# Kernel tuning notes

Measured on AMD Instinct MI355X. Metric: run time of the kernel, lower is better.

The kernel has to match this reference:

```python
import jax, jax.numpy as jnp
import numpy as np

D_MODEL = 1024
N_HEADS = 16
D_K = D_MODEL // N_HEADS
D_HIDDEN = 2048
LN_EPS = 1e-5


def setup_inputs() -> dict:
    key = jax.random.key(0)
    ks = jax.random.split(key, 16)
    s = 0.02
    inp = {
        'x': jax.random.normal(ks[0], (4, 2048, D_MODEL), dtype=jnp.float32),
        'Wq': jax.random.normal(ks[1], (D_MODEL, D_MODEL), dtype=jnp.float32) * s,
        'bq': jnp.zeros((D_MODEL,), jnp.float32),
        'Wk': jax.random.normal(ks[2], (D_MODEL, D_MODEL), dtype=jnp.float32) * s,
        'bk': jnp.zeros((D_MODEL,), jnp.float32),
        'Wv': jax.random.normal(ks[3], (D_MODEL, D_MODEL), dtype=jnp.float32) * s,
        'bv': jnp.zeros((D_MODEL,), jnp.float32),
        'Wo': jax.random.normal(ks[4], (D_MODEL, D_MODEL), dtype=jnp.float32) * s,
        'bo': jnp.zeros((D_MODEL,), jnp.float32),
        'ln1_g': jnp.ones((D_MODEL,), jnp.float32),
        'ln1_b': jnp.zeros((D_MODEL,), jnp.float32),
        'ln2_g': jnp.ones((D_MODEL,), jnp.float32),
        'ln2_b': jnp.zeros((D_MODEL,), jnp.float32),
        'W1': jax.random.normal(ks[5], (2 * D_HIDDEN, D_MODEL), dtype=jnp.float32) * s,
        'b1': jnp.zeros((2 * D_HIDDEN,), jnp.float32),
        'W2': jax.random.normal(ks[6], (D_MODEL, D_HIDDEN), dtype=jnp.float32) * s,
        'b2': jnp.zeros((D_MODEL,), jnp.float32),
    }
    return inp


def _layernorm(x, g, b):
    mu = jnp.mean(x, axis=-1, keepdims=True)
    var = jnp.mean(jnp.square(x - mu), axis=-1, keepdims=True)
    return (x - mu) * jax.lax.rsqrt(var + LN_EPS) * g + b


def _attention(xn, Wq, bq, Wk, bk, Wv, bv, Wo, bo):
    B, S, _ = xn.shape
    def split_heads(t):  # [B,S,D] -> [B,H,S,Dk]
        return t.reshape(B, S, N_HEADS, D_K).transpose(0, 2, 1, 3)
    Q = split_heads(xn @ Wq.T + bq)
    K = split_heads(xn @ Wk.T + bk)
    V = split_heads(xn @ Wv.T + bv)
    scores = jnp.einsum('bhqd,bhkd->bhqk', Q, K) / jnp.float32(D_K ** 0.5)
    attn = jax.nn.softmax(scores, axis=-1)  # torch code does max-sub + softmax (same math)
    ctx = jnp.einsum('bhqk,bhkd->bhqd', attn, V)
    ctx = ctx.transpose(0, 2, 1, 3).reshape(B, S, D_MODEL)
    return ctx @ Wo.T + bo


def reference(x, Wq, bq, Wk, bk, Wv, bv, Wo, bo, ln1_g, ln1_b, ln2_g, ln2_b, W1, b1, W2, b2):
    # pre-norm attention block
    xn = _layernorm(x, ln1_g, ln1_b)
    x = x + _attention(xn, Wq, bq, Wk, bk, Wv, bv, Wo, bo)
    # pre-norm ReGLU FFN
    xn = _layernorm(x, ln2_g, ln2_b)
    h = xn @ W1.T + b1
    a, b_ = jnp.split(h, 2, axis=-1)
    h = jax.nn.relu(a) * b_
    x = x + (h @ W2.T + b2)
    return x
```

## Files before the change

kernel.cpp:

```cpp
#include <hip/hip_runtime.h>
#include <hip/hip_bf16.h>

typedef __attribute__((ext_vector_type(8))) short short8;
typedef __attribute__((ext_vector_type(4))) float floatx4;

#define LN_EPS 1e-5f
#define EXP2_SCALE 0.18033688011112042f

__device__ __forceinline__ float b2f(unsigned short u) {
    union { float f; unsigned int i; } x; x.i = ((unsigned int)u) << 16; return x.f;
}
__device__ __forceinline__ unsigned short f2b(float f) {
    union { float f; unsigned int i; } x; x.f = f;
    unsigned int r = x.i + 0x7fffu + ((x.i >> 16) & 1u);
    return (unsigned short)(r >> 16);
}
__device__ __forceinline__ float to_f(unsigned short u) { return b2f(u); }
__device__ __forceinline__ float to_f(float f) { return f; }
__device__ __forceinline__ unsigned int pk_bf16(float a, float b) {
    union { float f; unsigned int i; } xa, xb; xa.f = a; xb.f = b;
    return (xa.i >> 16) | (xb.i & 0xffff0000u);
}

__device__ __forceinline__ void async16(const unsigned short* g, unsigned short* l) {
    __builtin_amdgcn_global_load_lds(
        (const __attribute__((address_space(1))) unsigned int*)g,
        (__attribute__((address_space(3))) unsigned int*)l, 16, 0, 0);
}

template<typename T>
__device__ __forceinline__ void ln_row(const T* __restrict__ xr, const float* __restrict__ g,
                                       const float* __restrict__ bb, unsigned short* __restrict__ outr,
                                       float* red)
{
    const int tid = threadIdx.x;
    float v[4];
#pragma unroll
    for (int i = 0; i < 4; i++) v[i] = to_f(xr[tid + i * 256]);
    float s  = v[0] + v[1] + v[2] + v[3];
    float sq = v[0]*v[0] + v[1]*v[1] + v[2]*v[2] + v[3]*v[3];
#pragma unroll
    for (int o = 32; o >= 1; o >>= 1) {
        s  += __shfl_xor(s,  o, 64);
        sq += __shfl_xor(sq, o, 64);
    }
    const int wave = tid >> 6, lane = tid & 63;
    if (lane == 0) { red[wave] = s; red[4 + wave] = sq; }
    __syncthreads();
    s  = red[0] + red[1] + red[2] + red[3];
    sq = red[4] + red[5] + red[6] + red[7];
    const float mu  = s * (1.0f / 1024.0f);
    const float var = sq * (1.0f / 1024.0f) - mu * mu;
    const float rs  = rsqrtf(var + LN_EPS);
#pragma unroll
    for (int i = 0; i < 4; i++) {
        int c = tid + i * 256;
        outr[c] = f2b((v[i] - mu) * rs * g[c] + bb[c]);
    }
}

__global__ __launch_bounds__(256)
void prep_kernel(const float* __restrict__ Wq, const float* __restrict__ Wk,
                 const float* __restrict__ Wv, const float* __restrict__ Wo,
                 const float* __restrict__ W1, const float* __restrict__ W2,
                 unsigned short* __restrict__ wdst,
                 const float* __restrict__ x, const float* __restrict__ ln1g,
                 const float* __restrict__ ln1b, unsigned short* __restrict__ xn)
{
    __shared__ float red[8];
    if (blockIdx.x < 5120) {
        const size_t i = (size_t)(blockIdx.x * 256 + threadIdx.x) * 8;
        const float* src; size_t off;
        if (i < 4194304) {
            int w = (int)(i >> 20);
            src = (w == 0) ? Wq : (w == 1) ? Wk : (w == 2) ? Wv : Wo;
            off = i & 1048575;
        } else if (i < 8388608) { src = W1; off = i - 4194304; }
        else                    { src = W2; off = i - 8388608; }
        float4 a = *reinterpret_cast<const float4*>(src + off);
        float4 b = *reinterpret_cast<const float4*>(src + off + 4);
        short8 r;
        r[0] = (short)f2b(a.x); r[1] = (short)f2b(a.y);
        r[2] = (short)f2b(a.z); r[3] = (short)f2b(a.w);
        r[4] = (short)f2b(b.x); r[5] = (short)f2b(b.y);
        r[6] = (short)f2b(b.z); r[7] = (short)f2b(b.w);
        *reinterpret_cast<short8*>(wdst + i) = r;
    } else {
        const int row = blockIdx.x - 5120;
        ln_row<float>(x + (size_t)row * 1024, ln1g, ln1b, xn + (size_t)row * 1024, red);
    }
}

__global__ __launch_bounds__(256)
void ln_kernel(const unsigned short* __restrict__ x, const float* __restrict__ g,
               const float* __restrict__ bb, unsigned short* __restrict__ out)
{
    __shared__ float red[8];
    const int row = blockIdx.x;
    ln_row<unsigned short>(x + (size_t)row * 1024, g, bb, out + (size_t)row * 1024, red);
}

template<int EPI>
__global__ __launch_bounds__(256, 3)
void gemm_nt(const unsigned short* __restrict__ A, const unsigned short* __restrict__ B,
             const float* __restrict__ bias, const void* __restrict__ res,
             void* __restrict__ C, int M, int N, int K)
{
    __shared__ unsigned short As[128 * 64];
    __shared__ unsigned short Bs[128 * 64];
    const int m0 = blockIdx.y * 128, n0 = blockIdx.x * 128;
    const int tid = threadIdx.x, wave = tid >> 6, lane = tid & 63;
    const int wm = (wave >> 1) * 64, wn = (wave & 1) * 64;
    const int lrow = lane & 15, quad = lane >> 4;
    const int srow = wave * 32 + (lane >> 3);
    const int scol = (((lane & 7) ^ ((lane >> 3) & 7)) << 3);
    const int ca0 = (quad ^ (lrow & 7)) << 3;
    const int ca1 = ((quad + 4) ^ (lrow & 7)) << 3;

    floatx4 acc[4][4] = {};
    const unsigned short* gA = A + (size_t)(m0 + srow) * K + scol;
    const unsigned short* gB = B + (size_t)(n0 + srow) * K + scol;
    unsigned short* lA = &As[(wave * 32) * 64];
    unsigned short* lB = &Bs[(wave * 32) * 64];

    for (int k0 = 0; k0 < K; k0 += 64) {
        __syncthreads();
#pragma unroll
        for (int r = 0; r < 4; r++) {
            async16(gA + k0 + (size_t)(r * 8) * K, lA + r * 8 * 64);
            async16(gB + k0 + (size_t)(r * 8) * K, lB + r * 8 * 64);
        }
        __syncthreads();
#pragma unroll
        for (int ks = 0; ks < 2; ks++) {
            const int ca = ks ? ca1 : ca0;
            short8 af[4], bf[4];
#pragma unroll
            for (int i = 0; i < 4; i++)
                af[i] = *reinterpret_cast<const short8*>(&As[(wm + i * 16 + lrow) * 64 + ca]);
#pragma unroll
            for (int j = 0; j < 4; j++)
                bf[j] = *reinterpret_cast<const short8*>(&Bs[(wn + j * 16 + lrow) * 64 + ca]);
#pragma unroll
            for (int i = 0; i < 4; i++)
#pragma unroll
                for (int j = 0; j < 4; j++)
                    acc[i][j] = __builtin_amdgcn_mfma_f32_16x16x32_bf16(af[i], bf[j], acc[i][j], 0, 0, 0);
        }
    }

#pragma unroll
    for (int i = 0; i < 4; i++) {
        int rb = m0 + wm + i * 16 + quad * 4;
#pragma unroll
        for (int j = 0; j < 4; j++) {
            int col = n0 + wn + j * 16 + lrow;
            float bv = bias[col];
#pragma unroll
            for (int r = 0; r < 4; r++) {
                size_t idx = (size_t)(rb + r) * N + col;
                float v = acc[i][j][r] + bv;
                if (EPI == 1) {
                    v += ((const float*)res)[idx];
                    ((unsigned short*)C)[idx] = f2b(v);
                } else {
                    v += b2f(((const unsigned short*)res)[idx]);
                    ((float*)C)[idx] = v;
                }
            }
        }
    }
}

__global__ __launch_bounds__(256, 3)
void gemm_qkv(const unsigned short* __restrict__ A, const unsigned short* __restrict__ Wqkv,
              const float* __restrict__ bq, const float* __restrict__ bk, const float* __restrict__ bv,
              unsigned short* __restrict__ QK, unsigned short* __restrict__ Vt)
{
    __shared__ unsigned short As[128 * 64];
    __shared__ unsigned short Bs[128 * 64];
    const int part = blockIdx.x >> 3;
    const int m0 = blockIdx.y * 128, n0 = (blockIdx.x & 7) * 128;
    const int tid = threadIdx.x, wave = tid >> 6, lane = tid & 63;
    const int wm = (wave >> 1) * 64, wn = (wave & 1) * 64;
    const int lrow = lane & 15, quad = lane >> 4;
    const int srow = wave * 32 + (lane >> 3);
    const int scol = (((lane & 7) ^ ((lane >> 3) & 7)) << 3);
    const int ca0 = (quad ^ (lrow & 7)) << 3;
    const int ca1 = ((quad + 4) ^ (lrow & 7)) << 3;
    const unsigned short* B = Wqkv + (size_t)part * 1048576;
    const float* bias = (part == 0) ? bq : (part == 1) ? bk : bv;

    floatx4 acc[4][4] = {};
    const unsigned short* gA = A + (size_t)(m0 + srow) * 1024 + scol;
    const unsigned short* gB = B + (size_t)(n0 + srow) * 1024 + scol;
    unsigned short* lA = &As[(wave * 32) * 64];
    unsigned short* lB = &Bs[(wave * 32) * 64];

    for (int k0 = 0; k0 < 1024; k0 += 64) {
        __syncthreads();
#pragma unroll
        for (int r = 0; r < 4; r++) {
            async16(gA + k0 + (size_t)(r * 8) * 1024, lA + r * 8 * 64);
            async16(gB + k0 + (size_t)(r * 8) * 1024, lB + r * 8 * 64);
        }
        __syncthreads();
#pragma unroll
        for (int ks = 0; ks < 2; ks++) {
            const int ca = ks ? ca1 : ca0;
            short8 af[4], bf[4];
#pragma unroll
            for (int i = 0; i < 4; i++)
                af[i] = *reinterpret_cast<const short8*>(&As[(wm + i * 16 + lrow) * 64 + ca]);
#pragma unroll
            for (int j = 0; j < 4; j++)
                bf[j] = *reinterpret_cast<const short8*>(&Bs[(wn + j * 16 + lrow) * 64 + ca]);
#pragma unroll
            for (int i = 0; i < 4; i++)
#pragma unroll
                for (int j = 0; j < 4; j++)
                    acc[i][j] = __builtin_amdgcn_mfma_f32_16x16x32_bf16(af[i], bf[j], acc[i][j], 0, 0, 0);
        }
    }

#pragma unroll
    for (int i = 0; i < 4; i++) {
        int rb = m0 + wm + i * 16 + quad * 4;
#pragma unroll
        for (int j = 0; j < 4; j++) {
            int col = n0 + wn + j * 16 + lrow;
            float bv2 = bias[col];
            if (part == 0) {
#pragma unroll
                for (int r = 0; r < 4; r++)
                    QK[(size_t)(rb + r) * 1024 + col] = f2b((acc[i][j][r] + bv2) * EXP2_SCALE);
            } else if (part == 1) {
                unsigned short* dst = QK + 8388608;
#pragma unroll
                for (int r = 0; r < 4; r++)
                    dst[(size_t)(rb + r) * 1024 + col] = f2b(acc[i][j][r] + bv2);
            } else {
                int b = rb >> 11, spos = rb & 2047;
                int h = col >> 6, d = col & 63;
                unsigned short* dst = Vt + (((size_t)(b * 16 + h) * 64 + d) << 11) + spos;
                unsigned int u01 = pk_bf16(acc[i][j][0] + bv2, acc[i][j][1] + bv2);
                u01 = (unsigned int)f2b(acc[i][j][0] + bv2) | ((unsigned int)f2b(acc[i][j][1] + bv2) << 16);
                unsigned int u23 = (unsigned int)f2b(acc[i][j][2] + bv2) | ((unsigned int)f2b(acc[i][j][3] + bv2) << 16);
                *reinterpret_cast<uint2*>(dst) = make_uint2(u01, u23);
            }
        }
    }
}

__global__ __launch_bounds__(256, 2)
void gemm_w1_reglu(const unsigned short* __restrict__ A, const unsigned short* __restrict__ B,
                   const float* __restrict__ bias, unsigned short* __restrict__ G)
{
    __shared__ unsigned short As[128 * 64];
    __shared__ unsigned short B0s[128 * 64];
    __shared__ unsigned short B1s[128 * 64];
    const int m0 = blockIdx.y * 128, n0 = blockIdx.x * 128;
    const int tid = threadIdx.x, wave = tid >> 6, lane = tid & 63;
    const int wm = (wave >> 1) * 64, wn = (wave & 1) * 64;
    const int lrow = lane & 15, quad = lane >> 4;
    const int srow = wave * 32 + (lane >> 3);
    const int scol = (((lane & 7) ^ ((lane >> 3) & 7)) << 3);
    const int ca0 = (quad ^ (lrow & 7)) << 3;
    const int ca1 = ((quad + 4) ^ (lrow & 7)) << 3;

    floatx4 acca[4][4] = {};
    floatx4 accb[4][4] = {};
    const unsigned short* gA  = A + (size_t)(m0 + srow) * 1024 + scol;
    const unsigned short* gB0 = B + (size_t)(n0 + srow) * 1024 + scol;
    const unsigned short* gB1 = B + (size_t)(2048 + n0 + srow) * 1024 + scol;
    unsigned short* lA  = &As [(wave * 32) * 64];
    unsigned short* lB0 = &B0s[(wave * 32) * 64];
    unsigned short* lB1 = &B1s[(wave * 32) * 64];

    for (int k0 = 0; k0 < 1024; k0 += 64) {
        __syncthreads();
#pragma unroll
        for (int r = 0; r < 4; r++) {
            async16(gA  + k0 + (size_t)(r * 8) * 1024, lA  + r * 8 * 64);
            async16(gB0 + k0 + (size_t)(r * 8) * 1024, lB0 + r * 8 * 64);
            async16(gB1 + k0 + (size_t)(r * 8) * 1024, lB1 + r * 8 * 64);
        }
        __syncthreads();
#pragma unroll
        for (int ks = 0; ks < 2; ks++) {
            const int ca = ks ? ca1 : ca0;
            short8 af[4], b0[4], b1[4];
#pragma unroll
            for (int i = 0; i < 4; i++)
                af[i] = *reinterpret_cast<const short8*>(&As[(wm + i * 16 + lrow) * 64 + ca]);
#pragma unroll
            for (int j = 0; j < 4; j++) {
                b0[j] = *reinterpret_cast<const short8*>(&B0s[(wn + j * 16 + lrow) * 64 + ca]);
                b1[j] = *reinterpret_cast<const short8*>(&B1s[(wn + j * 16 + lrow) * 64 + ca]);
            }
#pragma unroll
            for (int i = 0; i < 4; i++)
#pragma unroll
                for (int j = 0; j < 4; j++) {
                    acca[i][j] = __builtin_amdgcn_mfma_f32_16x16x32_bf16(af[i], b0[j], acca[i][j], 0, 0, 0);
                    accb[i][j] = __builtin_amdgcn_mfma_f32_16x16x32_bf16(af[i], b1[j], accb[i][j], 0, 0, 0);
                }
        }
    }

#pragma unroll
    for (int i = 0; i < 4; i++) {
        int rb = m0 + wm + i * 16 + quad * 4;
#pragma unroll
        for (int j = 0; j < 4; j++) {
            int col = n0 + wn + j * 16 + lrow;
            float ba = bias[col], bb2 = bias[2048 + col];
#pragma unroll
            for (int r = 0; r < 4; r++) {
                float va = acca[i][j][r] + ba;
                float vb = accb[i][j][r] + bb2;
                G[(size_t)(rb + r) * 2048 + col] = f2b(fmaxf(va, 0.0f) * vb);
            }
        }
    }
}

__global__ __launch_bounds__(256, 4)
void attn_kernel(const unsigned short* __restrict__ Qm, const unsigned short* __restrict__ Km,
                 const unsigned short* __restrict__ Vt, unsigned short* __restrict__ ctx)
{
    __shared__ unsigned short Ks[64 * 64];
    __shared__ unsigned short Vs[64 * 64];
    __shared__ unsigned short Ps[4][32][72];

    const int tid = threadIdx.x, wave = tid >> 6, lane = tid & 63;
    const int lrow = lane & 15, quad = lane >> 4;
    const int qb = blockIdx.x, bh = blockIdx.y;
    const size_t base  = (size_t)(bh >> 4) * 2048 * 1024 + (size_t)(bh & 15) * 64;
    const size_t vbase = (size_t)bh * 131072;
    const int q0 = qb * 128 + wave * 32;
    const int g_sub = (lane >> 3);
    const int g_col = (((lane & 7) ^ (g_sub & 7)) << 3);
    const int ca0 = (quad ^ (lrow & 7)) << 3;
    const int ca1 = ((quad + 4) ^ (lrow & 7)) << 3;

    short8 qf[2][2];
#pragma unroll
    for (int m = 0; m < 2; m++) {
        const unsigned short* qp = Qm + base + (size_t)(q0 + m * 16 + lrow) * 1024 + quad * 8;
        qf[m][0] = *reinterpret_cast<const short8*>(qp);
        qf[m][1] = *reinterpret_cast<const short8*>(qp + 32);
    }

    floatx4 o[2][4] = {};
    float li[2] = {0.f, 0.f};

    for (int t = 0; t < 32; t++) {
        const int k0 = t * 64;
        __syncthreads();
#pragma unroll
        for (int r = 0; r < 2; r++) {
            int krow = wave * 16 + r * 8 + g_sub;
            async16(Km + base + (size_t)(k0 + krow) * 1024 + g_col, &Ks[(wave * 16 + r * 8) * 64]);
            async16(Vt + vbase + (size_t)krow * 2048 + k0 + g_col,  &Vs[(wave * 16 + r * 8) * 64]);
        }
        __syncthreads();

        short8 kf0[4], kf1[4];
#pragma unroll
        for (int j = 0; j < 4; j++) {
            kf0[j] = *reinterpret_cast<const short8*>(&Ks[(j * 16 + lrow) * 64 + ca0]);
            kf1[j] = *reinterpret_cast<const short8*>(&Ks[(j * 16 + lrow) * 64 + ca1]);
        }
        floatx4 s4t[2][4] = {};
#pragma unroll
        for (int m = 0; m < 2; m++)
#pragma unroll
            for (int j = 0; j < 4; j++) {
                s4t[m][j] = __builtin_amdgcn_mfma_f32_16x16x32_bf16(kf0[j], qf[m][0], s4t[m][j], 0, 0, 0);
                s4t[m][j] = __builtin_amdgcn_mfma_f32_16x16x32_bf16(kf1[j], qf[m][1], s4t[m][j], 0, 0, 0);
            }

#pragma unroll
        for (int m = 0; m < 2; m++) {
            float acc = 0.f;
#pragma unroll
            for (int j = 0; j < 4; j++) {
                float p0 = __builtin_amdgcn_exp2f(s4t[m][j][0]);
                float p1 = __builtin_amdgcn_exp2f(s4t[m][j][1]);
                float p2 = __builtin_amdgcn_exp2f(s4t[m][j][2]);
                float p3 = __builtin_amdgcn_exp2f(s4t[m][j][3]);
                acc += (p0 + p1) + (p2 + p3);
                uint2 pk = make_uint2(pk_bf16(p0, p1), pk_bf16(p2, p3));
                *reinterpret_cast<uint2*>(&Ps[wave][m * 16 + lrow][j * 16 + quad * 4]) = pk;
            }
            li[m] += acc;
        }
        __asm__ volatile("s_waitcnt lgkmcnt(0)" ::: "memory");

        short8 pf[2][2];
#pragma unroll
        for (int m = 0; m < 2; m++) {
            pf[m][0] = *reinterpret_cast<const short8*>(&Ps[wave][m * 16 + lrow][quad * 8]);
            pf[m][1] = *reinterpret_cast<const short8*>(&Ps[wave][m * 16 + lrow][32 + quad * 8]);
        }
#pragma unroll
        for (int jj = 0; jj < 4; jj++) {
            short8 vf0 = *reinterpret_cast<const short8*>(&Vs[(jj * 16 + lrow) * 64 + ca0]);
            short8 vf1 = *reinterpret_cast<const short8*>(&Vs[(jj * 16 + lrow) * 64 + ca1]);
#pragma unroll
            for (int m = 0; m < 2; m++) {
                o[m][jj] = __builtin_amdgcn_mfma_f32_16x16x32_bf16(pf[m][0], vf0, o[m][jj], 0, 0, 0);
                o[m][jj] = __builtin_amdgcn_mfma_f32_16x16x32_bf16(pf[m][1], vf1, o[m][jj], 0, 0, 0);
            }
        }
    }

#pragma unroll
    for (int m = 0; m < 2; m++) {
        float l = li[m];
        l += __shfl_xor(l, 16, 64);
        l += __shfl_xor(l, 32, 64);
        float inv = 1.0f / l;
#pragma unroll
        for (int r = 0; r < 4; r++) {
            float invr = __shfl(inv, quad * 4 + r, 64);
            int srow = q0 + m * 16 + quad * 4 + r;
#pragma unroll
            for (int jj = 0; jj < 4; jj++)
                ctx[base + (size_t)srow * 1024 + jj * 16 + lrow] = f2b(o[m][jj][r] * invr);
        }
    }
}

extern "C" void kernel_launch(void* const* d_in, const int* in_sizes, int n_in,
                              void* d_out, int out_size, void* d_ws, size_t ws_size,
                              hipStream_t stream) {
    const float* x    = (const float*)d_in[0];
    const float* Wq   = (const float*)d_in[1];
    const float* bq   = (const float*)d_in[2];
    const float* Wk   = (const float*)d_in[3];
    const float* bk   = (const float*)d_in[4];
    const float* Wv   = (const float*)d_in[5];
    const float* bv   = (const float*)d_in[6];
    const float* Wo   = (const float*)d_in[7];
    const float* bo   = (const float*)d_in[8];
    const float* ln1g = (const float*)d_in[9];
    const float* ln1b = (const float*)d_in[10];
    const float* ln2g = (const float*)d_in[11];
    const float* ln2b = (const float*)d_in[12];
    const float* W1   = (const float*)d_in[13];
    const float* b1   = (const float*)d_in[14];
    const float* W2   = (const float*)d_in[15];
    const float* b2   = (const float*)d_in[16];
    float* out = (float*)d_out;

    char* ws = (char*)d_ws;
    unsigned short* wflat = (unsigned short*)ws;
    unsigned short* wqb = wflat;
    unsigned short* wob = wflat + 3145728;
    unsigned short* w1b = wflat + 4194304;
    unsigned short* w2b = wflat + 8388608;
    unsigned short* xn  = (unsigned short*)(ws + 20971520);
    unsigned short* Qm  = (unsigned short*)(ws + 37748736);
    unsigned short* x1b = (unsigned short*)(ws + 37748736);
    unsigned short* Vt  = (unsigned short*)(ws + 71303168);
    unsigned short* g   = (unsigned short*)(ws + 71303168);

    dim3 blk(256);
    prep_kernel<<<13312, blk, 0, stream>>>(Wq, Wk, Wv, Wo, W1, W2, wflat, x, ln1g, ln1b, xn);
    gemm_qkv<<<dim3(24, 64), blk, 0, stream>>>(xn, wqb, bq, bk, bv, Qm, Vt);
    attn_kernel<<<dim3(16, 64), blk, 0, stream>>>(Qm, Qm + 8388608, Vt, xn);
    gemm_nt<1><<<dim3(8, 64), blk, 0, stream>>>(xn, wob, bo, x, x1b, 8192, 1024, 1024);
    ln_kernel<<<8192, blk, 0, stream>>>(x1b, ln2g, ln2b, xn);
    gemm_w1_reglu<<<dim3(16, 64), blk, 0, stream>>>(xn, w1b, b1, g);
    gemm_nt<2><<<dim3(8, 64), blk, 0, stream>>>(g, w2b, b2, x1b, out, 8192, 1024, 2048);
}
```

Measured before the change: 437.9 us.

## Double-buffer K/V tiles in attention kernel with async prefetch and block swizzle

The attention kernel now keeps two K/V tile buffers in LDS. It prefetches the next 64-key tile with async loads while the current one is computed, replacing the two full syncthreads per iteration with vmcnt waits and s_barrier. It also remaps block indices so that nearby blocks share batch-head groups, and it raises wave priority around the MFMA sections. The doubled LDS use cuts the occupancy target from 4 to 3 blocks per CU, which may reduce latency hiding elsewhere. A redundant pk_bf16 call in the V write path is also dropped.

```diff
diff --git a/kernel.cpp b/kernel.cpp
--- a/kernel.cpp
+++ b/kernel.cpp
@@ -243,8 +243,7 @@
                 int b = rb >> 11, spos = rb & 2047;
                 int h = col >> 6, d = col & 63;
                 unsigned short* dst = Vt + (((size_t)(b * 16 + h) * 64 + d) << 11) + spos;
-                unsigned int u01 = pk_bf16(acc[i][j][0] + bv2, acc[i][j][1] + bv2);
-                u01 = (unsigned int)f2b(acc[i][j][0] + bv2) | ((unsigned int)f2b(acc[i][j][1] + bv2) << 16);
+                unsigned int u01 = (unsigned int)f2b(acc[i][j][0] + bv2) | ((unsigned int)f2b(acc[i][j][1] + bv2) << 16);
                 unsigned int u23 = (unsigned int)f2b(acc[i][j][2] + bv2) | ((unsigned int)f2b(acc[i][j][3] + bv2) << 16);
                 *reinterpret_cast<uint2*>(dst) = make_uint2(u01, u23);
             }
@@ -325,17 +324,19 @@
     }
 }
 
-__global__ __launch_bounds__(256, 4)
+__global__ __launch_bounds__(256, 3)
 void attn_kernel(const unsigned short* __restrict__ Qm, const unsigned short* __restrict__ Km,
                  const unsigned short* __restrict__ Vt, unsigned short* __restrict__ ctx)
 {
-    __shared__ unsigned short Ks[64 * 64];
-    __shared__ unsigned short Vs[64 * 64];
+    __shared__ unsigned short Ks[2][64 * 64];
+    __shared__ unsigned short Vs[2][64 * 64];
     __shared__ unsigned short Ps[4][32][72];
 
     const int tid = threadIdx.x, wave = tid >> 6, lane = tid & 63;
     const int lrow = lane & 15, quad = lane >> 4;
-    const int qb = blockIdx.x, bh = blockIdx.y;
+    const int id = blockIdx.x + (blockIdx.y << 4);
+    const int qb = id >> 6;
+    const int bh = ((id & 7) << 3) + ((id >> 3) & 7);
     const size_t base  = (size_t)(bh >> 4) * 2048 * 1024 + (size_t)(bh & 15) * 64;
     const size_t vbase = (size_t)bh * 131072;
     const int q0 = qb * 128 + wave * 32;
@@ -351,28 +352,29 @@
         qf[m][0] = *reinterpret_cast<const short8*>(qp);
         qf[m][1] = *reinterpret_cast<const short8*>(qp + 32);
     }
+    __asm__ volatile("s_waitcnt vmcnt(0)" ::: "memory");
 
     floatx4 o[2][4] = {};
     float li[2] = {0.f, 0.f};
 
-    for (int t = 0; t < 32; t++) {
-        const int k0 = t * 64;
-        __syncthreads();
+    auto stage = [&](int buf, int k0) {
 #pragma unroll
         for (int r = 0; r < 2; r++) {
             int krow = wave * 16 + r * 8 + g_sub;
-            async16(Km + base + (size_t)(k0 + krow) * 1024 + g_col, &Ks[(wave * 16 + r * 8) * 64]);
-            async16(Vt + vbase + (size_t)krow * 2048 + k0 + g_col,  &Vs[(wave * 16 + r * 8) * 64]);
-        }
-        __syncthreads();
-
+            async16(Km + base + (size_t)(k0 + krow) * 1024 + g_col, &Ks[buf][(wave * 16 + r * 8) * 64]);
+            async16(Vt + vbase + (size_t)krow * 2048 + k0 + g_col,  &Vs[buf][(wave * 16 + r * 8) * 64]);
+        }
+    };
+
+    auto compute = [&](int buf) {
         short8 kf0[4], kf1[4];
 #pragma unroll
         for (int j = 0; j < 4; j++) {
-            kf0[j] = *reinterpret_cast<const short8*>(&Ks[(j * 16 + lrow) * 64 + ca0]);
-            kf1[j] = *reinterpret_cast<const short8*>(&Ks[(j * 16 + lrow) * 64 + ca1]);
+            kf0[j] = *reinterpret_cast<const short8*>(&Ks[buf][(j * 16 + lrow) * 64 + ca0]);
+            kf1[j] = *reinterpret_cast<const short8*>(&Ks[buf][(j * 16 + lrow) * 64 + ca1]);
         }
         floatx4 s4t[2][4] = {};
+        __builtin_amdgcn_s_setprio(1);
 #pragma unroll
         for (int m = 0; m < 2; m++)
 #pragma unroll
@@ -380,6 +382,7 @@
                 s4t[m][j] = __builtin_amdgcn_mfma_f32_16x16x32_bf16(kf0[j], qf[m][0], s4t[m][j], 0, 0, 0);
                 s4t[m][j] = __builtin_amdgcn_mfma_f32_16x16x32_bf16(kf1[j], qf[m][1], s4t[m][j], 0, 0, 0);
             }
+        __builtin_amdgcn_s_setprio(0);
 
 #pragma unroll
         for (int m = 0; m < 2; m++) {
@@ -404,17 +407,37 @@
             pf[m][0] = *reinterpret_cast<const short8*>(&Ps[wave][m * 16 + lrow][quad * 8]);
             pf[m][1] = *reinterpret_cast<const short8*>(&Ps[wave][m * 16 + lrow][32 + quad * 8]);
         }
+        short8 vf0[4], vf1[4];
 #pragma unroll
         for (int jj = 0; jj < 4; jj++) {
-            short8 vf0 = *reinterpret_cast<const short8*>(&Vs[(jj * 16 + lrow) * 64 + ca0]);
-            short8 vf1 = *reinterpret_cast<const short8*>(&Vs[(jj * 16 + lrow) * 64 + ca1]);
+            vf0[jj] = *reinterpret_cast<const short8*>(&Vs[buf][(jj * 16 + lrow) * 64 + ca0]);
+            vf1[jj] = *reinterpret_cast<const short8*>(&Vs[buf][(jj * 16 + lrow) * 64 + ca1]);
+        }
+        __builtin_amdgcn_s_setprio(1);
+#pragma unroll
+        for (int jj = 0; jj < 4; jj++)
 #pragma unroll
             for (int m = 0; m < 2; m++) {
-                o[m][jj] = __builtin_amdgcn_mfma_f32_16x16x32_bf16(pf[m][0], vf0, o[m][jj], 0, 0, 0);
-                o[m][jj] = __builtin_amdgcn_mfma_f32_16x16x32_bf16(pf[m][1], vf1, o[m][jj], 0, 0, 0);
-            }
-        }
-    }
+                o[m][jj] = __builtin_amdgcn_mfma_f32_16x16x32_bf16(pf[m][0], vf0[jj], o[m][jj], 0, 0, 0);
+                o[m][jj] = __builtin_amdgcn_mfma_f32_16x16x32_bf16(pf[m][1], vf1[jj], o[m][jj], 0, 0, 0);
+            }
+        __builtin_amdgcn_s_setprio(0);
+    };
+
+    stage(0, 0);
+    for (int t = 0; t < 31; t++) {
+        stage((t + 1) & 1, (t + 1) << 6);
+        __asm__ volatile("s_waitcnt vmcnt(4)" ::: "memory");
+        __builtin_amdgcn_s_barrier();
+        __builtin_amdgcn_sched_barrier(0);
+        compute(t & 1);
+        __builtin_amdgcn_sched_barrier(0);
+        __builtin_amdgcn_s_barrier();
+    }
+    __asm__ volatile("s_waitcnt vmcnt(0)" ::: "memory");
+    __builtin_amdgcn_s_barrier();
+    __builtin_amdgcn_sched_barrier(0);
+    compute(1);
 
 #pragma unroll
     for (int m = 0; m < 2; m++) {
```

After: 441.2 us. Within noise of the previous version (+0.8%).
